# Optimization experiments

Hardware: AMD Instinct MI355X
Metric: run time of the kernel (lower is better)

The kernel has to match this reference:

```python
import jax, jax.numpy as jnp
import numpy as np

N_VARS = 16
BATCH = 16
SEQ = 512
P = N_VARS * (N_VARS - 1)  # ordered pairs i != j


def setup_inputs() -> dict:
    key = jax.random.key(0)
    ks = jax.random.split(key, 12)
    n = N_VARS

    def w(k, shape, fan_in):
        return jax.random.normal(k, shape, dtype=jnp.float32) / np.sqrt(fan_in)

    z = lambda *s: jnp.zeros(s, jnp.float32)
    return {
        'data': jax.random.normal(ks[0], (BATCH, SEQ, n), dtype=jnp.float32),
        # structure learner: n*n -> 256 -> 128 -> n*n (dropout skipped / eval mode)
        'Ws1': w(ks[1], (n * n, 256), n * n), 'bs1': z(256),
        'Ws2': w(ks[2], (256, 128), 256), 'bs2': z(128),
        'Ws3': w(ks[3], (128, n * n), 128), 'bs3': z(n * n),
        # per-variable causal mechanisms (stacked): (n-1) -> 128 -> 64 -> 1
        'Wm1': w(ks[4], (n, n - 1, 128), n - 1), 'bm1': z(n, 128),
        'Wm2': w(ks[5], (n, 128, 64), 128), 'bm2': z(n, 64),
        'Wm3': w(ks[6], (n, 64), 64), 'bm3': z(n),
        # per-pair independence tests (stacked): 2 -> 32 -> 1, sigmoid
        'Wt1': w(ks[7], (P, 2, 32), 2), 'bt1': z(P, 32),
        'Wt2': w(ks[8], (P, 32), 32), 'bt2': z(P),
    }


def reference(data, Ws1, bs1, Ws2, bs2, Ws3, bs3,
              Wm1, bm1, Wm2, bm2, Wm3, bm3,
              Wt1, bt1, Wt2, bt2):
    B, S, n = data.shape
    N = B * S
    flat = data.reshape(N, n)  # [N, n] all samples

    # ---- correlations of batch-averaged series (vectorized corrcoef) ----
    avg = data.mean(axis=0)                    # [S, n]
    xc = avg - avg.mean(axis=0, keepdims=True)
    cov = xc.T @ xc                            # [n, n]
    std = jnp.sqrt(jnp.clip(jnp.diag(cov), 0.0))
    denom = std[:, None] * std[None, :]
    corr = jnp.abs(jnp.where(denom > 0, cov / jnp.where(denom > 0, denom, 1.0), 0.0))
    corr = corr * (1.0 - jnp.eye(n, dtype=corr.dtype))  # zero diagonal (i != j only)

    # ---- structure learner MLP -> sigmoid -> strict upper-tri DAG mask ----
    h = jax.nn.relu(corr.reshape(1, -1) @ Ws1 + bs1)
    h = jax.nn.relu(h @ Ws2 + bs2)
    adj = jax.nn.sigmoid(h @ Ws3 + bs3).reshape(n, n)
    adj = jnp.triu(adj, 1)

    # ---- causal mechanisms: gather-parents -> per-var MLP -> scatter ----
    idx = np.stack([[j for j in range(n) if j != v] for v in range(n)])  # [n, n-1]
    pmask = adj > 0.5
    parent_mask = pmask[idx, np.arange(n)[:, None]].astype(flat.dtype)   # [n, n-1]
    inp = flat[:, idx] * parent_mask[None]                               # [N, n, n-1]
    h1 = jax.nn.relu(jnp.einsum('nvp,vph->nvh', inp, Wm1) + bm1)         # [N, n, 128]
    h2 = jax.nn.relu(jnp.einsum('nvh,vhk->nvk', h1, Wm2) + bm2)          # [N, n, 64]
    mech = jnp.einsum('nvk,vk->nv', h2, Wm3) + bm3                       # [N, n]
    has_parents = parent_mask.sum(axis=1) > 0                            # [n]
    predictions = jnp.where(has_parents[None, :], mech, flat).reshape(B, S, n)

    # ---- batched per-pair independence tests ----
    pairs = np.array([(i, j) for i in range(n) for j in range(n) if i != j])
    pi, pj = pairs[:, 0], pairs[:, 1]
    X = jnp.stack([flat[:, pi], flat[:, pj]], axis=-1)                   # [N, P, 2]
    ht = jax.nn.relu(jnp.einsum('npc,pch->nph', X, Wt1) + bt1)           # [N, P, 32]
    s = jax.nn.sigmoid(jnp.einsum('nph,ph->np', ht, Wt2) + bt2).mean(axis=0)  # [P]
    scores = jnp.zeros((n, n), flat.dtype).at[pi, pj].set(s)

    return adj, predictions, scores
```

## Files before the change

### kernel.cpp

```cpp
#include <hip/hip_runtime.h>
#include <hip/hip_bf16.h>


typedef __attribute__((ext_vector_type(8))) short bf16x8;
typedef __attribute__((ext_vector_type(4))) short bf16x4;
typedef __attribute__((ext_vector_type(4))) float f32x4;

#define DEV __device__ __forceinline__
DEV short f2bf(float f){ __hip_bfloat16 h = __float2bfloat16(f); short s; __builtin_memcpy(&s,&h,2); return s; }
DEV float bf2f(short s){ __hip_bfloat16 h; __builtin_memcpy(&h,&s,2); return __bfloat162float(h); }

#define WS_P1(b)   ((b)*272)
#define WS_SCORES  8704
#define WS_PM      8960
#define WS_HP      9200
#define WS_DUMMY   9400
#define WS_FLAG    9600
#define FLAG_MAGIC 0x1357F00D

__global__ void __launch_bounds__(512) k_main(
    const float* __restrict__ data,
    const float* __restrict__ Ws1, const float* __restrict__ bs1,
    const float* __restrict__ Ws2, const float* __restrict__ bs2,
    const float* __restrict__ Ws3, const float* __restrict__ bs3,
    const float* __restrict__ Wt1, const float* __restrict__ bt1,
    const float* __restrict__ Wt2, const float* __restrict__ bt2,
    float* __restrict__ wsf, float* __restrict__ out)
{
    __shared__ float sh[2048];
    __shared__ float av[16*17];
    int tid = threadIdx.x;
    int* flags = (int*)(wsf + WS_FLAG);

    if (blockIdx.x != 0) {
        int p = blockIdx.x - 1;

        if (blockIdx.x <= 32) {
            int b = blockIdx.x - 1;
            if (tid < 256) {
                int sl = tid >> 4, vv = tid & 15;
                int s = b*16 + sl;
                float acc = 0.f;
                #pragma unroll
                for (int bt = 0; bt < 16; ++bt) acc += data[bt*8192 + s*16 + vv];
                av[sl*17 + vv] = acc * (1.f/16.f);
            }
            __syncthreads();
            if (tid < 256) {
                int i = tid >> 4, j = tid & 15;
                float p1 = 0.f;
                #pragma unroll
                for (int r = 0; r < 16; ++r) p1 += av[r*17 + i] * av[r*17 + j];
                wsf[WS_P1(b) + tid] = p1;
            }
            if (tid < 16) {
                float ms = 0.f;
                #pragma unroll
                for (int r = 0; r < 16; ++r) ms += av[r*17 + tid];
                wsf[WS_P1(b) + 256 + tid] = ms;
            }
            unsigned xr = 0;
            { uint4 u = ((const uint4*)Ws1)[b*512 + tid]; xr ^= u.x^u.y^u.z^u.w; }
            if (tid < 256) { uint4 u = ((const uint4*)Ws2)[b*256 + tid];       xr ^= u.x^u.y^u.z^u.w; }
            else           { uint4 u = ((const uint4*)Ws3)[b*256 + tid - 256]; xr ^= u.x^u.y^u.z^u.w; }
            if (xr == 0x9E3779B9u) wsf[WS_DUMMY] = 0.f;
            __syncthreads();
            if (tid == 0) {
                __threadfence();
                __hip_atomic_store(&flags[b], FLAG_MAGIC,
                                   __ATOMIC_RELEASE, __HIP_MEMORY_SCOPE_AGENT);
            }
        }

        int i = p / 15, jr = p % 15;
        int j = jr + (jr >= i ? 1 : 0);
        float* w0 = sh;        float* w1 = sh + 32;
        float* bb = sh + 64;   float* w2 = sh + 96;
        float* red = sh + 128;
        if (tid < 32) {
            w0[tid] = Wt1[p*64 + tid];
            w1[tid] = Wt1[p*64 + 32 + tid];
            bb[tid] = bt1[p*32 + tid];
            w2[tid] = Wt2[p*32 + tid];
        }
        if (tid == 0) sh[700] = bt2[p];
        __syncthreads();
        float b2s = sh[700];
        float acc = 0.f;
        for (int it = 0; it < 16; ++it) {
            int s = it*512 + tid;
            float xa = data[s*16 + i];
            float xb = data[s*16 + j];
            float z = b2s;
            #pragma unroll
            for (int h = 0; h < 32; ++h) {
                float t1 = fmaf(xa, w0[h], fmaf(xb, w1[h], bb[h]));
                z = fmaf(fmaxf(t1, 0.f), w2[h], z);
            }
            acc += 1.f / (1.f + expf(-z));
        }
        red[tid] = acc;
        __syncthreads();
        for (int off = 256; off > 0; off >>= 1) {
            if (tid < off) red[tid] += red[tid + off];
            __syncthreads();
        }
        if (tid == 0) wsf[WS_SCORES + p] = red[0] * (1.f/8192.f);
        return;
    }

    if (tid < 32) {
        while (__hip_atomic_load(&flags[tid], __ATOMIC_ACQUIRE,
                                 __HIP_MEMORY_SCOPE_AGENT) != FLAG_MAGIC)
            __builtin_amdgcn_s_sleep(2);
    }
    __syncthreads();
    __threadfence();

    float* corr_s = sh;          float* part   = sh + 256;
    float* h1_s   = sh + 768;    float* h2_s   = sh + 1024;
    float* adj_s  = sh + 1152;   float* pm_s   = sh + 1408;
    float* m_s    = sh + 1648;   float* std_s  = sh + 1664;
    float* cov_s  = sh + 1680;

    float p1 = 0.f;
    if (tid < 256) { for (int b = 0; b < 32; ++b) p1 += wsf[WS_P1(b) + tid]; }
    if (tid < 16) {
        float ms = 0.f;
        for (int b = 0; b < 32; ++b) ms += wsf[WS_P1(b) + 256 + tid];
        m_s[tid] = ms * (1.f/512.f);
    }
    __syncthreads();
    if (tid < 256) { int i = tid>>4, j = tid&15; cov_s[tid] = p1 - 512.f*m_s[i]*m_s[j]; }
    __syncthreads();
    if (tid < 16) std_s[tid] = sqrtf(fmaxf(cov_s[tid*17], 0.f));
    __syncthreads();
    if (tid < 256) {
        int i = tid>>4, j = tid&15;
        float den = std_s[i]*std_s[j];
        corr_s[tid] = (den > 0.f && i != j) ? fabsf(cov_s[tid]/den) : 0.f;
    }
    __syncthreads();
    {
        int t = tid & 255, half = tid >> 8;
        float a = 0.f;
        #pragma unroll 8
        for (int i = half*128; i < half*128 + 128; ++i)
            a = fmaf(corr_s[i], Ws1[i*256 + t], a);
        part[half*256 + t] = a;
    }
    __syncthreads();
    if (tid < 256) h1_s[tid] = fmaxf(part[tid] + part[256 + tid] + bs1[tid], 0.f);
    __syncthreads();
    {
        int t = tid & 127, qq = tid >> 7;
        float a = 0.f;
        #pragma unroll 8
        for (int i = qq*64; i < qq*64 + 64; ++i)
            a = fmaf(h1_s[i], Ws2[i*128 + t], a);
        part[qq*128 + t] = a;
    }
    __syncthreads();
    if (tid < 128)
        h2_s[tid] = fmaxf(part[tid] + part[128+tid] + part[256+tid] + part[384+tid] + bs2[tid], 0.f);
    __syncthreads();
    {
        int t = tid & 255, half = tid >> 8;
        float a = 0.f;
        #pragma unroll 8
        for (int i = half*64; i < half*64 + 64; ++i)
            a = fmaf(h2_s[i], Ws3[i*256 + t], a);
        part[half*256 + t] = a;
    }
    __syncthreads();
    if (tid < 256) {
        float z = part[tid] + part[256 + tid] + bs3[tid];
        float a = 1.f / (1.f + expf(-z));
        int r = tid >> 4, cc = tid & 15;
        float adjv = (r < cc) ? a : 0.f;
        adj_s[tid] = adjv;
        out[tid] = adjv;
    }
    __syncthreads();
    if (tid < 240) {
        int v = tid / 15, pr = tid % 15;
        int jj = pr + (pr >= v ? 1 : 0);
        float pmv = (adj_s[jj*16 + v] > 0.5f) ? 1.f : 0.f;
        wsf[WS_PM + tid] = pmv;
        pm_s[tid] = pmv;
    }
    __syncthreads();
    if (tid < 16) {
        float sum = 0.f;
        #pragma unroll
        for (int pr = 0; pr < 15; ++pr) sum += pm_s[tid*15 + pr];
        wsf[WS_HP + tid] = (sum > 0.f) ? 1.f : 0.f;
    }
}

__global__ void __launch_bounds__(256, 2) k_mech(
    const float* __restrict__ data,
    const float* __restrict__ Wm1, const float* __restrict__ bm1,
    const float* __restrict__ Wm2, const float* __restrict__ bm2,
    const float* __restrict__ Wm3, const float* __restrict__ bm3,
    const float* __restrict__ wsf, float* __restrict__ out)
{
    int tid = threadIdx.x, bid = blockIdx.x;
    int v = bid >> 5, chunk = bid & 31;
    int gs0 = chunk * 256;

    __shared__ __align__(16) short smX[256*24];
    __shared__ __align__(16) short smW2T[64*136];
    __shared__ __align__(16) short smH1[4][16*136];
    __shared__ __align__(16) float smW1[16*128];
    __shared__ __align__(16) float smB1[128];
    __shared__ float smB2[64];
    __shared__ float smW3[64];

    for (int e = tid; e < 2048; e += 256) {
        int k = e >> 7, h = e & 127;
        float val = 0.f;
        if (k != v) {
            int p = k - (k > v ? 1 : 0);
            val = Wm1[v*1920 + p*128 + h] * wsf[WS_PM + v*15 + p];
        }
        smW1[e] = val;
    }
    for (int e = tid; e < 8192; e += 256) {
        int h = e >> 6, j = e & 63;
        smW2T[j*136 + h] = f2bf(Wm2[v*8192 + e]);
    }
    for (int e = tid; e < 4096; e += 256) {
        int s = e >> 4, k = e & 15;
        smX[s*24 + k] = f2bf(data[gs0*16 + e]);
    }
    if (tid < 128) smB1[tid] = bm1[v*128 + tid];
    else if (tid < 192) smB2[tid - 128] = bm2[v*64 + tid - 128];
    else smW3[tid - 192] = Wm3[v*64 + tid - 192];
    __syncthreads();

    int lane = tid & 63, wid = tid >> 6;
    int c = lane & 15, q = lane >> 4;
    float hp = wsf[WS_HP + v];
    float bm3v = bm3[v];

    bf16x8 a1[8];
    #pragma unroll
    for (int ht = 0; ht < 8; ++ht) {
        #pragma unroll
        for (int jj = 0; jj < 8; ++jj) {
            int k = q*8 + jj;
            float w = (k < 16) ? smW1[k*128 + ht*16 + c] : 0.f;
            a1[ht][jj] = f2bf(w);
        }
    }
    bf16x8 b2r[16];
    #pragma unroll
    for (int jt = 0; jt < 4; ++jt)
        #pragma unroll
        for (int ks = 0; ks < 4; ++ks)
            b2r[jt*4 + ks] = *(const bf16x8*)&smW2T[(jt*16 + c)*136 + ks*32 + q*8];
    float w3c[4], b2c[4];
    #pragma unroll
    for (int jt = 0; jt < 4; ++jt) { w3c[jt] = smW3[jt*16 + c]; b2c[jt] = smB2[jt*16 + c]; }

    short* h1buf = smH1[wid];

    for (int stl = 0; stl < 4; ++stl) {
        int st = wid*4 + stl;
        bf16x8 xb;
        #pragma unroll
        for (int i2 = 0; i2 < 8; ++i2) xb[i2] = 0;
        if (q < 2) xb = *(const bf16x8*)&smX[(st*16 + c)*24 + q*8];
        f32x4 c1[8];
        #pragma unroll
        for (int ht = 0; ht < 8; ++ht) c1[ht] = *(const f32x4*)&smB1[ht*16 + q*4];
        #pragma unroll
        for (int ht = 0; ht < 8; ++ht)
            c1[ht] = __builtin_amdgcn_mfma_f32_16x16x32_bf16(a1[ht], xb, c1[ht], 0, 0, 0);
        #pragma unroll
        for (int ht = 0; ht < 8; ++ht) {
            bf16x4 pk;
            #pragma unroll
            for (int r = 0; r < 4; ++r) pk[r] = f2bf(fmaxf(c1[ht][r], 0.f));
            *(bf16x4*)&h1buf[c*136 + ht*16 + q*4] = pk;
        }
        f32x4 c2[4];
        #pragma unroll
        for (int jt = 0; jt < 4; ++jt) {
            float bi = b2c[jt];
            c2[jt] = (f32x4){bi, bi, bi, bi};
        }
        #pragma unroll
        for (int ks = 0; ks < 4; ++ks) {
            bf16x8 a2 = *(const bf16x8*)&h1buf[c*136 + ks*32 + q*8];
            #pragma unroll
            for (int jt = 0; jt < 4; ++jt)
                c2[jt] = __builtin_amdgcn_mfma_f32_16x16x32_bf16(a2, b2r[jt*4 + ks], c2[jt], 0, 0, 0);
        }
        float part[4];
        #pragma unroll
        for (int r = 0; r < 4; ++r) part[r] = 0.f;
        #pragma unroll
        for (int jt = 0; jt < 4; ++jt)
            #pragma unroll
            for (int r = 0; r < 4; ++r)
                part[r] = fmaf(fmaxf(c2[jt][r], 0.f), w3c[jt], part[r]);
        #pragma unroll
        for (int off = 1; off < 16; off <<= 1)
            #pragma unroll
            for (int r = 0; r < 4; ++r)
                part[r] += __shfl_xor(part[r], off, 16);
        if (c == 0) {
            #pragma unroll
            for (int r = 0; r < 4; ++r) {
                int s_loc = st*16 + q*4 + r;
                float mech = part[r] + bm3v;
                float xv = bf2f(smX[s_loc*24 + v]);
                out[256 + (gs0 + s_loc)*16 + v] = (hp != 0.f) ? mech : xv;
            }
        }
    }

    if (bid == 0 && tid < 256) {
        int i = tid >> 4, j = tid & 15;
        float s = 0.f;
        if (i != j) s = wsf[WS_SCORES + i*15 + j - (j > i ? 1 : 0)];
        out[256 + 131072 + tid] = s;
    }
}

extern "C" void kernel_launch(void* const* d_in, const int* in_sizes, int n_in,
                              void* d_out, int out_size, void* d_ws, size_t ws_size,
                              hipStream_t stream)
{
    const float* data = (const float*)d_in[0];
    const float* Ws1  = (const float*)d_in[1];
    const float* bs1  = (const float*)d_in[2];
    const float* Ws2  = (const float*)d_in[3];
    const float* bs2  = (const float*)d_in[4];
    const float* Ws3  = (const float*)d_in[5];
    const float* bs3  = (const float*)d_in[6];
    const float* Wm1  = (const float*)d_in[7];
    const float* bm1  = (const float*)d_in[8];
    const float* Wm2  = (const float*)d_in[9];
    const float* bm2  = (const float*)d_in[10];
    const float* Wm3  = (const float*)d_in[11];
    const float* bm3  = (const float*)d_in[12];
    const float* Wt1  = (const float*)d_in[13];
    const float* bt1  = (const float*)d_in[14];
    const float* Wt2  = (const float*)d_in[15];
    const float* bt2  = (const float*)d_in[16];
    float* wsf = (float*)d_ws;
    float* out = (float*)d_out;

    hipLaunchKernelGGL(k_main, dim3(241), dim3(512), 0, stream,
                       data, Ws1, bs1, Ws2, bs2, Ws3, bs3,
                       Wt1, bt1, Wt2, bt2, wsf, out);
    hipLaunchKernelGGL(k_mech, dim3(512), dim3(256), 0, stream,
                       data, Wm1, bm1, Wm2, bm2, Wm3, bm3, wsf, out);
}
```

Before: 119.5 us.

## Fuse mechanism kernel into main kernel with flag-based cross-block synchronization

Merges the two launches into one 753-block kernel. Mechanism blocks stage weights and data into shared memory, then spin on a flag that block 0 publishes after computing the DAG mask, so their setup overlaps the structure-learner chain. The parent mask is now applied in-register to the W1 fragments, and the pair blocks write scores directly to the output. Blocks shrink to 256 threads and the small MLP loops use four accumulators, but spin-waiting blocks could deadlock or stall if block 0 is not scheduled early, and flags are never reset between calls.

```diff
diff --git a/kernel.cpp b/kernel.cpp
--- a/kernel.cpp
+++ b/kernel.cpp
@@ -11,84 +11,229 @@
 DEV float bf2f(short s){ __hip_bfloat16 h; __builtin_memcpy(&h,&s,2); return __bfloat162float(h); }
 
 #define WS_P1(b)   ((b)*272)
-#define WS_SCORES  8704
 #define WS_PM      8960
 #define WS_HP      9200
 #define WS_DUMMY   9400
 #define WS_FLAG    9600
 #define FLAG_MAGIC 0x1357F00D
 
-__global__ void __launch_bounds__(512) k_main(
+union SMem {
+    struct {
+        float sh[2048];
+        float av[16*17];
+    } g;
+    struct {
+        short X[256*24];
+        short W2T[64*136];
+        short H1[4*16*136];
+        short W1[16*128];
+        float B1[128];
+        float B2[64];
+        float W3[64];
+        float PMk[17];
+    } m;
+};
+
+__global__ void __launch_bounds__(256) k_all(
     const float* __restrict__ data,
     const float* __restrict__ Ws1, const float* __restrict__ bs1,
     const float* __restrict__ Ws2, const float* __restrict__ bs2,
     const float* __restrict__ Ws3, const float* __restrict__ bs3,
+    const float* __restrict__ Wm1, const float* __restrict__ bm1,
+    const float* __restrict__ Wm2, const float* __restrict__ bm2,
+    const float* __restrict__ Wm3, const float* __restrict__ bm3,
     const float* __restrict__ Wt1, const float* __restrict__ bt1,
     const float* __restrict__ Wt2, const float* __restrict__ bt2,
     float* __restrict__ wsf, float* __restrict__ out)
 {
-    __shared__ float sh[2048];
-    __shared__ float av[16*17];
-    int tid = threadIdx.x;
+    __shared__ __align__(16) SMem sm;
+    int tid = threadIdx.x, bid = blockIdx.x;
     int* flags = (int*)(wsf + WS_FLAG);
 
-    if (blockIdx.x != 0) {
-        int p = blockIdx.x - 1;
-
-        if (blockIdx.x <= 32) {
-            int b = blockIdx.x - 1;
-            if (tid < 256) {
-                int sl = tid >> 4, vv = tid & 15;
-                int s = b*16 + sl;
-                float acc = 0.f;
-                #pragma unroll
-                for (int bt = 0; bt < 16; ++bt) acc += data[bt*8192 + s*16 + vv];
-                av[sl*17 + vv] = acc * (1.f/16.f);
-            }
+    if (bid >= 241) {
+        int vid = bid - 241;
+        int v = vid >> 5, chunk = vid & 31;
+        int gs0 = chunk * 256;
+
+        for (int e = tid; e < 2048; e += 256) {
+            int k = e >> 7, h = e & 127;
+            float val = 0.f;
+            if (k != v) {
+                int p = k - (k > v ? 1 : 0);
+                val = Wm1[v*1920 + p*128 + h];
+            }
+            sm.m.W1[e] = f2bf(val);
+        }
+        for (int e = tid; e < 8192; e += 256) {
+            int h = e >> 6, j = e & 63;
+            sm.m.W2T[j*136 + h] = f2bf(Wm2[v*8192 + e]);
+        }
+        for (int e = tid; e < 4096; e += 256) {
+            int s = e >> 4, k = e & 15;
+            sm.m.X[s*24 + k] = f2bf(data[gs0*16 + e]);
+        }
+        if (tid < 128) sm.m.B1[tid] = bm1[v*128 + tid];
+        else if (tid < 192) sm.m.B2[tid - 128] = bm2[v*64 + tid - 128];
+        else sm.m.W3[tid - 192] = Wm3[v*64 + tid - 192];
+        float bm3v = bm3[v];
+        __syncthreads();
+
+        int lane = tid & 63, wid = tid >> 6;
+        int c = lane & 15, q = lane >> 4;
+
+        bf16x8 b2r[16];
+        #pragma unroll
+        for (int jt = 0; jt < 4; ++jt)
+            #pragma unroll
+            for (int ks = 0; ks < 4; ++ks)
+                b2r[jt*4 + ks] = *(const bf16x8*)&sm.m.W2T[(jt*16 + c)*136 + ks*32 + q*8];
+        float w3c[4], b2c[4];
+        #pragma unroll
+        for (int jt = 0; jt < 4; ++jt) { w3c[jt] = sm.m.W3[jt*16 + c]; b2c[jt] = sm.m.B2[jt*16 + c]; }
+
+        while (__hip_atomic_load(&flags[32], __ATOMIC_ACQUIRE,
+                                 __HIP_MEMORY_SCOPE_AGENT) != FLAG_MAGIC)
+            __builtin_amdgcn_s_sleep(2);
+        if (tid < 16) {
+            int k = tid;
+            sm.m.PMk[k] = (k == v) ? 0.f
+                        : wsf[WS_PM + v*15 + k - (k > v ? 1 : 0)];
+        }
+        if (tid == 16) sm.m.PMk[16] = wsf[WS_HP + v];
+        __syncthreads();
+        float hp = sm.m.PMk[16];
+
+        bf16x8 a1[8];
+        #pragma unroll
+        for (int ht = 0; ht < 8; ++ht) {
+            #pragma unroll
+            for (int jj = 0; jj < 8; ++jj) {
+                int k = q*8 + jj;
+                float w = (k < 16) ? bf2f(sm.m.W1[k*128 + ht*16 + c]) * sm.m.PMk[k] : 0.f;
+                a1[ht][jj] = f2bf(w);
+            }
+        }
+
+        short* h1buf = sm.m.H1 + wid*16*136;
+        for (int stl = 0; stl < 4; ++stl) {
+            int st = wid*4 + stl;
+            bf16x8 xb;
+            #pragma unroll
+            for (int i2 = 0; i2 < 8; ++i2) xb[i2] = 0;
+            if (q < 2) xb = *(const bf16x8*)&sm.m.X[(st*16 + c)*24 + q*8];
+            f32x4 c1[8];
+            #pragma unroll
+            for (int ht = 0; ht < 8; ++ht) c1[ht] = *(const f32x4*)&sm.m.B1[ht*16 + q*4];
+            #pragma unroll
+            for (int ht = 0; ht < 8; ++ht)
+                c1[ht] = __builtin_amdgcn_mfma_f32_16x16x32_bf16(a1[ht], xb, c1[ht], 0, 0, 0);
+            #pragma unroll
+            for (int ht = 0; ht < 8; ++ht) {
+                bf16x4 pk;
+                #pragma unroll
+                for (int r = 0; r < 4; ++r) pk[r] = f2bf(fmaxf(c1[ht][r], 0.f));
+                *(bf16x4*)&h1buf[c*136 + ht*16 + q*4] = pk;
+            }
+            f32x4 c2[4];
+            #pragma unroll
+            for (int jt = 0; jt < 4; ++jt) {
+                float bi = b2c[jt];
+                c2[jt] = (f32x4){bi, bi, bi, bi};
+            }
+            #pragma unroll
+            for (int ks = 0; ks < 4; ++ks) {
+                bf16x8 a2 = *(const bf16x8*)&h1buf[c*136 + ks*32 + q*8];
+                #pragma unroll
+                for (int jt = 0; jt < 4; ++jt)
+                    c2[jt] = __builtin_amdgcn_mfma_f32_16x16x32_bf16(a2, b2r[jt*4 + ks], c2[jt], 0, 0, 0);
+            }
+            float part[4];
+            #pragma unroll
+            for (int r = 0; r < 4; ++r) part[r] = 0.f;
+            #pragma unroll
+            for (int jt = 0; jt < 4; ++jt)
+                #pragma unroll
+                for (int r = 0; r < 4; ++r)
+                    part[r] = fmaf(fmaxf(c2[jt][r], 0.f), w3c[jt], part[r]);
+            #pragma unroll
+            for (int off = 1; off < 16; off <<= 1)
+                #pragma unroll
+                for (int r = 0; r < 4; ++r)
+                    part[r] += __shfl_xor(part[r], off, 16);
+            if (c == 0) {
+                #pragma unroll
+                for (int r = 0; r < 4; ++r) {
+                    int s_loc = st*16 + q*4 + r;
+                    float mech = part[r] + bm3v;
+                    float xv = bf2f(sm.m.X[s_loc*24 + v]);
+                    out[256 + (gs0 + s_loc)*16 + v] = (hp != 0.f) ? mech : xv;
+                }
+            }
+        }
+        return;
+    }
+
+    if (bid != 0) {
+        int p = bid - 1;
+
+        if (bid <= 32) {
+            int b = bid - 1;
+            int sl = tid >> 4, vv = tid & 15;
+            int s = b*16 + sl;
+            float acc = 0.f;
+            #pragma unroll
+            for (int bt = 0; bt < 16; ++bt) acc += data[bt*8192 + s*16 + vv];
+            sm.g.av[sl*17 + vv] = acc * (1.f/16.f);
             __syncthreads();
-            if (tid < 256) {
+            {
                 int i = tid >> 4, j = tid & 15;
                 float p1 = 0.f;
                 #pragma unroll
-                for (int r = 0; r < 16; ++r) p1 += av[r*17 + i] * av[r*17 + j];
+                for (int r = 0; r < 16; ++r) p1 += sm.g.av[r*17 + i] * sm.g.av[r*17 + j];
                 wsf[WS_P1(b) + tid] = p1;
             }
             if (tid < 16) {
                 float ms = 0.f;
                 #pragma unroll
-                for (int r = 0; r < 16; ++r) ms += av[r*17 + tid];
+                for (int r = 0; r < 16; ++r) ms += sm.g.av[r*17 + tid];
                 wsf[WS_P1(b) + 256 + tid] = ms;
             }
-            unsigned xr = 0;
-            { uint4 u = ((const uint4*)Ws1)[b*512 + tid]; xr ^= u.x^u.y^u.z^u.w; }
-            if (tid < 256) { uint4 u = ((const uint4*)Ws2)[b*256 + tid];       xr ^= u.x^u.y^u.z^u.w; }
-            else           { uint4 u = ((const uint4*)Ws3)[b*256 + tid - 256]; xr ^= u.x^u.y^u.z^u.w; }
-            if (xr == 0x9E3779B9u) wsf[WS_DUMMY] = 0.f;
             __syncthreads();
             if (tid == 0) {
                 __threadfence();
                 __hip_atomic_store(&flags[b], FLAG_MAGIC,
                                    __ATOMIC_RELEASE, __HIP_MEMORY_SCOPE_AGENT);
             }
+            unsigned xr = 0;
+            {
+                const uint4* w1 = (const uint4*)Ws1;
+                uint4 u = w1[b*512 + tid];        xr ^= u.x^u.y^u.z^u.w;
+                uint4 u2 = w1[b*512 + 256 + tid]; xr ^= u2.x^u2.y^u2.z^u2.w;
+                const uint4* w2 = (const uint4*)Ws2;
+                uint4 u3 = w2[b*256 + tid];       xr ^= u3.x^u3.y^u3.z^u3.w;
+                const uint4* w3 = (const uint4*)Ws3;
+                uint4 u4 = w3[b*256 + tid];       xr ^= u4.x^u4.y^u4.z^u4.w;
+            }
+            if (xr == 0x9E3779B9u) wsf[WS_DUMMY] = 0.f;
         }
 
         int i = p / 15, jr = p % 15;
         int j = jr + (jr >= i ? 1 : 0);
-        float* w0 = sh;        float* w1 = sh + 32;
-        float* bb = sh + 64;   float* w2 = sh + 96;
-        float* red = sh + 128;
+        float* w0 = sm.g.sh;        float* w1 = sm.g.sh + 32;
+        float* bb = sm.g.sh + 64;   float* w2 = sm.g.sh + 96;
+        float* red = sm.g.sh + 128;
         if (tid < 32) {
             w0[tid] = Wt1[p*64 + tid];
             w1[tid] = Wt1[p*64 + 32 + tid];
             bb[tid] = bt1[p*32 + tid];
             w2[tid] = Wt2[p*32 + tid];
         }
-        if (tid == 0) sh[700] = bt2[p];
-        __syncthreads();
-        float b2s = sh[700];
+        if (tid == 0) sm.g.sh[700] = bt2[p];
+        __syncthreads();
+        float b2s = sm.g.sh[700];
         float acc = 0.f;
-        for (int it = 0; it < 16; ++it) {
-            int s = it*512 + tid;
+        for (int it = 0; it < 32; ++it) {
+            int s = it*256 + tid;
             float xa = data[s*16 + i];
             float xb = data[s*16 + j];
             float z = b2s;
@@ -101,11 +246,11 @@
         }
         red[tid] = acc;
         __syncthreads();
-        for (int off = 256; off > 0; off >>= 1) {
+        for (int off = 128; off > 0; off >>= 1) {
             if (tid < off) red[tid] += red[tid + off];
             __syncthreads();
         }
-        if (tid == 0) wsf[WS_SCORES + p] = red[0] * (1.f/8192.f);
+        if (tid == 0) out[256 + 131072 + i*16 + j] = red[0] * (1.f/8192.f);
         return;
     }
 
@@ -117,64 +262,74 @@
     __syncthreads();
     __threadfence();
 
-    float* corr_s = sh;          float* part   = sh + 256;
-    float* h1_s   = sh + 768;    float* h2_s   = sh + 1024;
-    float* adj_s  = sh + 1152;   float* pm_s   = sh + 1408;
-    float* m_s    = sh + 1648;   float* std_s  = sh + 1664;
-    float* cov_s  = sh + 1680;
-
-    float p1 = 0.f;
-    if (tid < 256) { for (int b = 0; b < 32; ++b) p1 += wsf[WS_P1(b) + tid]; }
-    if (tid < 16) {
-        float ms = 0.f;
-        for (int b = 0; b < 32; ++b) ms += wsf[WS_P1(b) + 256 + tid];
-        m_s[tid] = ms * (1.f/512.f);
-    }
-    __syncthreads();
-    if (tid < 256) { int i = tid>>4, j = tid&15; cov_s[tid] = p1 - 512.f*m_s[i]*m_s[j]; }
+    float* corr_s = sm.g.sh;          float* part   = sm.g.sh + 256;
+    float* h1_s   = sm.g.sh + 768;    float* h2_s   = sm.g.sh + 1024;
+    float* adj_s  = sm.g.sh + 1152;   float* pm_s   = sm.g.sh + 1408;
+    float* m_s    = sm.g.sh + 1648;   float* std_s  = sm.g.sh + 1664;
+    float* cov_s  = sm.g.sh + 1680;
+
+    {
+        float p1 = 0.f;
+        #pragma unroll 8
+        for (int b = 0; b < 32; ++b) p1 += wsf[WS_P1(b) + tid];
+        if (tid < 16) {
+            float ms = 0.f;
+            #pragma unroll 8
+            for (int b = 0; b < 32; ++b) ms += wsf[WS_P1(b) + 256 + tid];
+            m_s[tid] = ms * (1.f/512.f);
+        }
+        __syncthreads();
+        int i = tid >> 4, j = tid & 15;
+        cov_s[tid] = p1 - 512.f*m_s[i]*m_s[j];
+    }
     __syncthreads();
     if (tid < 16) std_s[tid] = sqrtf(fmaxf(cov_s[tid*17], 0.f));
     __syncthreads();
-    if (tid < 256) {
-        int i = tid>>4, j = tid&15;
+    {
+        int i = tid >> 4, j = tid & 15;
         float den = std_s[i]*std_s[j];
         corr_s[tid] = (den > 0.f && i != j) ? fabsf(cov_s[tid]/den) : 0.f;
     }
     __syncthreads();
     {
-        int t = tid & 255, half = tid >> 8;
-        float a = 0.f;
+        float a0=0.f, a1=0.f, a2=0.f, a3=0.f;
         #pragma unroll 8
-        for (int i = half*128; i < half*128 + 128; ++i)
-            a = fmaf(corr_s[i], Ws1[i*256 + t], a);
-        part[half*256 + t] = a;
-    }
-    __syncthreads();
-    if (tid < 256) h1_s[tid] = fmaxf(part[tid] + part[256 + tid] + bs1[tid], 0.f);
-    __syncthreads();
-    {
-        int t = tid & 127, qq = tid >> 7;
-        float a = 0.f;
+        for (int i = 0; i < 256; i += 4) {
+            a0 = fmaf(corr_s[i  ], Ws1[(i  )*256 + tid], a0);
+            a1 = fmaf(corr_s[i+1], Ws1[(i+1)*256 + tid], a1);
+            a2 = fmaf(corr_s[i+2], Ws1[(i+2)*256 + tid], a2);
+            a3 = fmaf(corr_s[i+3], Ws1[(i+3)*256 + tid], a3);
+        }
+        h1_s[tid] = fmaxf(a0+a1+a2+a3 + bs1[tid], 0.f);
+    }
+    __syncthreads();
+    {
+        int t = tid & 127, half = tid >> 7;
+        const float* W2p = Ws2 + half*128*128;
+        const float* h1p = h1_s + half*128;
+        float a0=0.f, a1=0.f, a2=0.f, a3=0.f;
         #pragma unroll 8
-        for (int i = qq*64; i < qq*64 + 64; ++i)
-            a = fmaf(h1_s[i], Ws2[i*128 + t], a);
-        part[qq*128 + t] = a;
-    }
-    __syncthreads();
-    if (tid < 128)
-        h2_s[tid] = fmaxf(part[tid] + part[128+tid] + part[256+tid] + part[384+tid] + bs2[tid], 0.f);
-    __syncthreads();
-    {
-        int t = tid & 255, half = tid >> 8;
-        float a = 0.f;
+        for (int i = 0; i < 128; i += 4) {
+            a0 = fmaf(h1p[i  ], W2p[(i  )*128 + t], a0);
+            a1 = fmaf(h1p[i+1], W2p[(i+1)*128 + t], a1);
+            a2 = fmaf(h1p[i+2], W2p[(i+2)*128 + t], a2);
+            a3 = fmaf(h1p[i+3], W2p[(i+3)*128 + t], a3);
+        }
+        part[half*128 + t] = a0+a1+a2+a3;
+    }
+    __syncthreads();
+    if (tid < 128) h2_s[tid] = fmaxf(part[tid] + part[128 + tid] + bs2[tid], 0.f);
+    __syncthreads();
+    {
+        float a0=0.f, a1=0.f, a2=0.f, a3=0.f;
         #pragma unroll 8
-        for (int i = half*64; i < half*64 + 64; ++i)
-            a = fmaf(h2_s[i], Ws3[i*256 + t], a);
-        part[half*256 + t] = a;
-    }
-    __syncthreads();
-    if (tid < 256) {
-        float z = part[tid] + part[256 + tid] + bs3[tid];
+        for (int i = 0; i < 128; i += 4) {
+            a0 = fmaf(h2_s[i  ], Ws3[(i  )*256 + tid], a0);
+            a1 = fmaf(h2_s[i+1], Ws3[(i+1)*256 + tid], a1);
+            a2 = fmaf(h2_s[i+2], Ws3[(i+2)*256 + tid], a2);
+            a3 = fmaf(h2_s[i+3], Ws3[(i+3)*256 + tid], a3);
+        }
+        float z = a0+a1+a2+a3 + bs3[tid];
         float a = 1.f / (1.f + expf(-z));
         int r = tid >> 4, cc = tid & 15;
         float adjv = (r < cc) ? a : 0.f;
@@ -189,6 +344,7 @@
         wsf[WS_PM + tid] = pmv;
         pm_s[tid] = pmv;
     }
+    if (tid < 16) out[256 + 131072 + tid*17] = 0.f;
     __syncthreads();
     if (tid < 16) {
         float sum = 0.f;
@@ -196,137 +352,11 @@
         for (int pr = 0; pr < 15; ++pr) sum += pm_s[tid*15 + pr];
         wsf[WS_HP + tid] = (sum > 0.f) ? 1.f : 0.f;
     }
-}
-
-__global__ void __launch_bounds__(256, 2) k_mech(
-    const float* __restrict__ data,
-    const float* __restrict__ Wm1, const float* __restrict__ bm1,
-    const float* __restrict__ Wm2, const float* __restrict__ bm2,
-    const float* __restrict__ Wm3, const float* __restrict__ bm3,
-    const float* __restrict__ wsf, float* __restrict__ out)
-{
-    int tid = threadIdx.x, bid = blockIdx.x;
-    int v = bid >> 5, chunk = bid & 31;
-    int gs0 = chunk * 256;
-
-    __shared__ __align__(16) short smX[256*24];
-    __shared__ __align__(16) short smW2T[64*136];
-    __shared__ __align__(16) short smH1[4][16*136];
-    __shared__ __align__(16) float smW1[16*128];
-    __shared__ __align__(16) float smB1[128];
-    __shared__ float smB2[64];
-    __shared__ float smW3[64];
-
-    for (int e = tid; e < 2048; e += 256) {
-        int k = e >> 7, h = e & 127;
-        float val = 0.f;
-        if (k != v) {
-            int p = k - (k > v ? 1 : 0);
-            val = Wm1[v*1920 + p*128 + h] * wsf[WS_PM + v*15 + p];
-        }
-        smW1[e] = val;
-    }
-    for (int e = tid; e < 8192; e += 256) {
-        int h = e >> 6, j = e & 63;
-        smW2T[j*136 + h] = f2bf(Wm2[v*8192 + e]);
-    }
-    for (int e = tid; e < 4096; e += 256) {
-        int s = e >> 4, k = e & 15;
-        smX[s*24 + k] = f2bf(data[gs0*16 + e]);
-    }
-    if (tid < 128) smB1[tid] = bm1[v*128 + tid];
-    else if (tid < 192) smB2[tid - 128] = bm2[v*64 + tid - 128];
-    else smW3[tid - 192] = Wm3[v*64 + tid - 192];
-    __syncthreads();
-
-    int lane = tid & 63, wid = tid >> 6;
-    int c = lane & 15, q = lane >> 4;
-    float hp = wsf[WS_HP + v];
-    float bm3v = bm3[v];
-
-    bf16x8 a1[8];
-    #pragma unroll
-    for (int ht = 0; ht < 8; ++ht) {
-        #pragma unroll
-        for (int jj = 0; jj < 8; ++jj) {
-            int k = q*8 + jj;
-            float w = (k < 16) ? smW1[k*128 + ht*16 + c] : 0.f;
-            a1[ht][jj] = f2bf(w);
-        }
-    }
-    bf16x8 b2r[16];
-    #pragma unroll
-    for (int jt = 0; jt < 4; ++jt)
-        #pragma unroll
-        for (int ks = 0; ks < 4; ++ks)
-            b2r[jt*4 + ks] = *(const bf16x8*)&smW2T[(jt*16 + c)*136 + ks*32 + q*8];
-    float w3c[4], b2c[4];
-    #pragma unroll
-    for (int jt = 0; jt < 4; ++jt) { w3c[jt] = smW3[jt*16 + c]; b2c[jt] = smB2[jt*16 + c]; }
-
-    short* h1buf = smH1[wid];
-
-    for (int stl = 0; stl < 4; ++stl) {
-        int st = wid*4 + stl;
-        bf16x8 xb;
-        #pragma unroll
-        for (int i2 = 0; i2 < 8; ++i2) xb[i2] = 0;
-        if (q < 2) xb = *(const bf16x8*)&smX[(st*16 + c)*24 + q*8];
-        f32x4 c1[8];
-        #pragma unroll
-        for (int ht = 0; ht < 8; ++ht) c1[ht] = *(const f32x4*)&smB1[ht*16 + q*4];
-        #pragma unroll
-        for (int ht = 0; ht < 8; ++ht)
-            c1[ht] = __builtin_amdgcn_mfma_f32_16x16x32_bf16(a1[ht], xb, c1[ht], 0, 0, 0);
-        #pragma unroll
-        for (int ht = 0; ht < 8; ++ht) {
-            bf16x4 pk;
-            #pragma unroll
-            for (int r = 0; r < 4; ++r) pk[r] = f2bf(fmaxf(c1[ht][r], 0.f));
-            *(bf16x4*)&h1buf[c*136 + ht*16 + q*4] = pk;
-        }
-        f32x4 c2[4];
-        #pragma unroll
-        for (int jt = 0; jt < 4; ++jt) {
-            float bi = b2c[jt];
-            c2[jt] = (f32x4){bi, bi, bi, bi};
-        }
-        #pragma unroll
-        for (int ks = 0; ks < 4; ++ks) {
-            bf16x8 a2 = *(const bf16x8*)&h1buf[c*136 + ks*32 + q*8];
-            #pragma unroll
-            for (int jt = 0; jt < 4; ++jt)
-                c2[jt] = __builtin_amdgcn_mfma_f32_16x16x32_bf16(a2, b2r[jt*4 + ks], c2[jt], 0, 0, 0);
-        }
-        float part[4];
-        #pragma unroll
-        for (int r = 0; r < 4; ++r) part[r] = 0.f;
-        #pragma unroll
-        for (int jt = 0; jt < 4; ++jt)
-            #pragma unroll
-            for (int r = 0; r < 4; ++r)
-                part[r] = fmaf(fmaxf(c2[jt][r], 0.f), w3c[jt], part[r]);
-        #pragma unroll
-        for (int off = 1; off < 16; off <<= 1)
-            #pragma unroll
-            for (int r = 0; r < 4; ++r)
-                part[r] += __shfl_xor(part[r], off, 16);
-        if (c == 0) {
-            #pragma unroll
-            for (int r = 0; r < 4; ++r) {
-                int s_loc = st*16 + q*4 + r;
-                float mech = part[r] + bm3v;
-                float xv = bf2f(smX[s_loc*24 + v]);
-                out[256 + (gs0 + s_loc)*16 + v] = (hp != 0.f) ? mech : xv;
-            }
-        }
-    }
-
-    if (bid == 0 && tid < 256) {
-        int i = tid >> 4, j = tid & 15;
-        float s = 0.f;
-        if (i != j) s = wsf[WS_SCORES + i*15 + j - (j > i ? 1 : 0)];
-        out[256 + 131072 + tid] = s;
+    __syncthreads();
+    if (tid == 0) {
+        __threadfence();
+        __hip_atomic_store(&flags[32], FLAG_MAGIC,
+                           __ATOMIC_RELEASE, __HIP_MEMORY_SCOPE_AGENT);
     }
 }
 
@@ -354,9 +384,8 @@
     float* wsf = (float*)d_ws;
     float* out = (float*)d_out;
 
-    hipLaunchKernelGGL(k_main, dim3(241), dim3(512), 0, stream,
+    hipLaunchKernelGGL(k_all, dim3(753), dim3(256), 0, stream,
                        data, Ws1, bs1, Ws2, bs2, Ws3, bs3,
+                       Wm1, bm1, Wm2, bm2, Wm3, bm3,
                        Wt1, bt1, Wt2, bt2, wsf, out);
-    hipLaunchKernelGGL(k_mech, dim3(512), dim3(256), 0, stream,
-                       data, Wm1, bm1, Wm2, bm2, Wm3, bm3, wsf, out);
 }
```

Result: slower. 290.7 us (+143.3%).
